# Kernel optimization log

Measured on AMD Instinct MI355X. Metric: run time of the kernel, lower is better.

The kernel has to match this reference:

```python
import jax, jax.numpy as jnp
import numpy as np

# Module constants (match init_kwargs)
M = 2049                      # NpointsMesh (odd)
TAU = 2.821e-5                # Gaussian spreading width ~ 12*(pi/M)^2
XLIMS = (0.0, 10.0)
L = abs(XLIMS[1] - XLIMS[0])
KGRID = jnp.asarray(np.linspace(-(M // 2), M // 2, M), dtype=jnp.float32)        # (M,)
XGRID = jnp.asarray(2.0 * np.pi * np.linspace(XLIMS[0], XLIMS[1], M + 1)[:-1] / L,
                    dtype=jnp.float32)                                           # (M,)
FOUR_PI = 4.0 * np.pi


def setup_inputs() -> dict:
    key = jax.random.key(0)
    kx, = jax.random.split(key, 1)
    x = jax.random.uniform(kx, (16, 1024), dtype=jnp.float32) * 10.0  # points in [xLims[0], xLims[1])
    ones = jnp.ones((1,), dtype=jnp.float32)  # tf.initializers.ones for all 4 weights
    return {"x": x, "shift0": ones, "amp0": ones, "shift1": ones, "amp1": ones}


def reference(x, shift0, amp0, shift1, amp1):
    # Gaussian spreading: (B, N, M)
    diff = x[..., None] * (2.0 * np.pi / L) - XGRID
    g = jnp.exp(-jnp.square(diff) / (4.0 * TAU))
    # Sum over points -> gridded density (B, M), then FFT + shift
    gsum = jnp.sum(g, axis=1).astype(jnp.complex64)
    fft_g = jnp.fft.fftshift(jnp.fft.fft(gsum, axis=-1), axes=-1) * (L / (2.0 * np.pi))
    # Deconvolution of the Gaussian kernel (real-valued)
    deconv = jnp.sqrt(np.pi / TAU) * jnp.exp(jnp.square(KGRID) * TAU)  # (M,)
    rfft = fft_g * deconv  # (B, M) complex
    # Fourier multipliers (real; imag parts are structurally zero in the original)
    m1 = -amp0 * FOUR_PI / (jnp.square(KGRID) + jnp.square(5.0 * shift0))            # (M,)
    m2 = amp1 * FOUR_PI * jnp.square(1.0 / (jnp.square(KGRID) + jnp.square(5.0 * shift1)))  # (M,)
    mult = jnp.stack([m1, m2], axis=0)  # (2, M)
    mult_fft = mult[None, :, :].astype(jnp.complex64) * rfft[:, None, :]  # (B, 2, M)
    mult_deconv = mult_fft * deconv  # second deconv application, as in the original
    # Inverse FFT back to the mesh, keep real part: (B, 2, M)
    irfft = jnp.real(jnp.fft.ifft(jnp.fft.ifftshift(mult_deconv, axes=-1), axis=-1))
    # Inverse interpolation back to the points: (B, N, 2, M) -> (B, N, 2)
    local = irfft[:, None, :, :] * g[:, :, None, :]
    fmm = jnp.sum(local, axis=-1) / M
    return fmm
```

## Files before the change

kernel.cpp:

```cpp
#include <hip/hip_runtime.h>
#include <math.h>

#define M_   2049
#define B_   16
#define N_   1024
#define TAU_ 2.821e-5
#define PI_  3.14159265358979323846
#define TWO_PI_ 6.283185307179586476925286766559

#define CV_SPLIT 16
#define MPAD     2052

#define GS_CH    8
#define HT_BLKS  33
#define FMM_QB   4

#define SW(i) ((i) + ((i) >> 2))

__global__ __launch_bounds__(256)
void spread_h3(const float* __restrict__ x,
               const float* __restrict__ s0, const float* __restrict__ a0,
               const float* __restrict__ s1, const float* __restrict__ a1,
               double* __restrict__ gsum_part, double* __restrict__ hhalf) {
    __shared__ double smem[4609];
    const int bx  = blockIdx.x;
    const int tid = threadIdx.x;

    if (bx < GS_CH * B_) {
        const int b  = bx >> 3;
        const int ch = bx & (GS_CH - 1);
        for (int i = tid; i < M_; i += 256) smem[i] = 0.0;
        __syncthreads();
        const int pl  = tid >> 1;
        const int sub = tid & 1;
        const double du      = TWO_PI_ / (double)M_;
        const double inv4tau = 1.0 / (4.0 * TAU_);
        const double xv = (double)x[(b << 10) + (ch << 7) + pl];
        const double u  = xv * (TWO_PI_ / 10.0);
        const int mc = (int)(xv * ((double)M_ / 10.0) + 0.5);
        const int start = mc - 33 + sub * 34;
        for (int i = 0; i < 34; ++i) {
            int m = start + i;
            if (m >= 0 && m < M_) {
                double d = u - du * (double)m;
                double t = d * d * inv4tau;
                if (t < 88.0) atomicAdd(&smem[m], (double)__expf(-(float)t));
            }
        }
        __syncthreads();
        double* gp = gsum_part + ((size_t)ch * B_ + b) * M_;
        for (int i = tid; i < M_; i += 256) gp[i] = smem[i];
    } else {
        const int dtile = bx - GS_CH * B_;
        double* costab = smem;
        double* cf0    = smem + 2049;
        double* cf1    = smem + 3073;
        double* red    = smem + 4097;
        const double ang0 = TWO_PI_ / (double)M_;
        for (int i = tid; i <= 1024; i += 256) {
            double v = cos(ang0 * (double)i);
            costab[i] = v;
            if (i > 0) costab[M_ - i] = v;
        }
        const double sA = 5.0 * (double)s0[0], sB = 5.0 * (double)s1[0];
        const double amp0 = (double)a0[0],     amp1 = (double)a1[0];
        for (int jj = tid; jj < 1024; jj += 256) {
            double j  = (double)(jj + 1);
            double k2 = j * j;
            double dec2 = (PI_ / TAU_) * exp(2.0 * TAU_ * k2);
            double base = 2.0 * (10.0 / TWO_PI_) * dec2 / (double)M_;
            cf0[jj] = base * (-amp0 * 4.0 * PI_ / (k2 + sA * sA));
            double den = k2 + sB * sB;
            cf1[jj] = base * (amp1 * 4.0 * PI_ / (den * den));
        }
        __syncthreads();
        const int dl = tid & 31;
        const int jq = tid >> 5;
        const int d  = (dtile << 5) + dl;
        double acc0 = 0.0, acc1 = 0.0;
        if (d <= 1024) {
            const int jlo = (jq << 7) + 1;
            int r = (int)(((long long)jlo * (long long)d) % M_);
            #pragma unroll 4
            for (int jj = 0; jj < 128; ++jj) {
                double cv_ = costab[r];
                acc0 += cf0[(jq << 7) + jj] * cv_;
                acc1 += cf1[(jq << 7) + jj] * cv_;
                r += d; if (r >= M_) r -= M_;
            }
        }
        red[tid]       = acc0;
        red[256 + tid] = acc1;
        __syncthreads();
        if (tid < 32) {
            const int dd = (dtile << 5) + tid;
            if (dd <= 1024) {
                const double w0base = (10.0 / TWO_PI_) * (PI_ / TAU_) / (double)M_;
                double h0 = w0base * (-amp0 * 4.0 * PI_ / (sA * sA));
                double h1 = w0base * (amp1 * 4.0 * PI_ / ((sB * sB) * (sB * sB)));
                #pragma unroll
                for (int q = 0; q < 8; ++q) {
                    h0 += red[(q << 5) + tid];
                    h1 += red[256 + (q << 5) + tid];
                }
                hhalf[dd]        = h0;
                hhalf[1025 + dd] = h1;
            }
        }
    }
}

__global__ void conv_kernel(const double* __restrict__ gsum_part,
                            const double* __restrict__ hhalf,
                            double* __restrict__ part) {
    __shared__ double w0s[1456];
    __shared__ double w1s[1456];
    __shared__ double red[512];
    __shared__ double gls[132];
    const int mt = blockIdx.x;
    const int s  = blockIdx.y;
    const int b  = blockIdx.z;
    const int m0  = mt * 1024;
    const int p0  = (s * M_) / CV_SPLIT;
    const int p1  = ((s + 1) * M_) / CV_SPLIT;
    const int len = p1 - p0;
    const int wcount = 1024 + len;
    int base = m0 - (p0 + len - 1);
    while (base < 0) base += M_;
    for (int i = threadIdx.x; i < wcount; i += 256) {
        int idx = base + i;
        while (idx >= M_) idx -= M_;
        int dd = (idx > 1024) ? (M_ - idx) : idx;
        w0s[SW(i)] = hhalf[dd];
        w1s[SW(i)] = hhalf[1025 + dd];
    }
    for (int i = threadIdx.x; i < len; i += 256) {
        double acc = 0.0;
        #pragma unroll
        for (int ch = 0; ch < GS_CH; ++ch)
            acc += gsum_part[((size_t)ch * B_ + b) * M_ + p0 + i];
        gls[i] = acc;
    }
    __syncthreads();

    const int q = 4 * threadIdx.x + len - 1;
    double A0 = w0s[SW(q)], A1 = w0s[SW(q+1)], A2 = w0s[SW(q+2)], A3 = w0s[SW(q+3)];
    double C0 = w1s[SW(q)], C1 = w1s[SW(q+1)], C2 = w1s[SW(q+2)], C3 = w1s[SW(q+3)];
    double a00=0.0,a01=0.0,a02=0.0,a03=0.0, a10=0.0,a11=0.0,a12=0.0,a13=0.0;
    int j = q, tt = 0;
    for (; tt + 4 <= len; tt += 4) {
        double g;
        g = gls[tt];
        a00 += g*A0; a01 += g*A1; a02 += g*A2; a03 += g*A3;
        a10 += g*C0; a11 += g*C1; a12 += g*C2; a13 += g*C3;
        A3 = w0s[SW(j-1)]; C3 = w1s[SW(j-1)];
        g = gls[tt+1];
        a00 += g*A3; a01 += g*A0; a02 += g*A1; a03 += g*A2;
        a10 += g*C3; a11 += g*C0; a12 += g*C1; a13 += g*C2;
        A2 = w0s[SW(j-2)]; C2 = w1s[SW(j-2)];
        g = gls[tt+2];
        a00 += g*A2; a01 += g*A3; a02 += g*A0; a03 += g*A1;
        a10 += g*C2; a11 += g*C3; a12 += g*C0; a13 += g*C1;
        A1 = w0s[SW(j-3)]; C1 = w1s[SW(j-3)];
        g = gls[tt+3];
        a00 += g*A1; a01 += g*A2; a02 += g*A3; a03 += g*A0;
        a10 += g*C1; a11 += g*C2; a12 += g*C3; a13 += g*C0;
        A0 = w0s[SW(j-4)]; C0 = w1s[SW(j-4)];
        j -= 4;
    }
    for (; tt < len; ++tt) {
        double g = gls[tt];
        a00 += g*A0; a01 += g*A1; a02 += g*A2; a03 += g*A3;
        a10 += g*C0; a11 += g*C1; a12 += g*C2; a13 += g*C3;
    }
    {
        double* pv = part + (((size_t)s * B_ + b) * 2) * MPAD + m0 + 4 * threadIdx.x;
        pv[0]        = a00; pv[1]        = a01; pv[2]        = a02; pv[3]        = a03;
        pv[MPAD + 0] = a10; pv[MPAD + 1] = a11; pv[MPAD + 2] = a12; pv[MPAD + 3] = a13;
    }
    if (mt == 1) {
        double t0 = 0.0, t1 = 0.0;
        if (threadIdx.x < len) {
            double g = gls[threadIdx.x];
            int qq = 1023 + len - threadIdx.x;
            t0 = g * w0s[SW(qq)];
            t1 = g * w1s[SW(qq)];
        }
        red[threadIdx.x]       = t0;
        red[256 + threadIdx.x] = t1;
        __syncthreads();
        for (int off = 128; off > 0; off >>= 1) {
            if (threadIdx.x < off) {
                red[threadIdx.x]       += red[threadIdx.x + off];
                red[256 + threadIdx.x] += red[256 + threadIdx.x + off];
            }
            __syncthreads();
        }
        if (threadIdx.x == 0) {
            double* pv = part + (((size_t)s * B_ + b) * 2) * MPAD;
            pv[2048]        = red[0];
            pv[MPAD + 2048] = red[256];
        }
    }
}

__global__ __launch_bounds__(256)
void reduce_fmm(const float* __restrict__ x, const double* __restrict__ part,
                float* __restrict__ out) {
    __shared__ double convs[2 * M_];
    const int b   = blockIdx.x >> 2;
    const int qb  = blockIdx.x & (FMM_QB - 1);
    const int tid = threadIdx.x;
    const size_t sstride = (size_t)B_ * 2 * MPAD;
    for (int ch = 0; ch < 2; ++ch) {
        const size_t off0 = ((size_t)b * 2 + ch) * MPAD;
        for (int m = tid; m < M_; m += 256) {
            double acc = 0.0;
            #pragma unroll
            for (int k = 0; k < CV_SPLIT; ++k)
                acc += part[(size_t)k * sstride + off0 + m];
            convs[ch * M_ + m] = acc;
        }
    }
    __syncthreads();
    const double du      = TWO_PI_ / (double)M_;
    const double inv4tau = 1.0 / (4.0 * TAU_);
    const int p  = (b << 10) + (qb << 8) + tid;
    const double xv = (double)x[p];
    const double u  = xv * (TWO_PI_ / 10.0);
    int mc = (int)(xv * ((double)M_ / 10.0) + 0.5);
    int lo = mc - 34; if (lo < 0) lo = 0;
    int hi = mc + 34; if (hi > M_ - 1) hi = M_ - 1;
    double av0 = 0.0, av1 = 0.0;
    for (int m = lo; m <= hi; ++m) {
        double d = u - du * (double)m;
        double g = (double)__expf(-(float)(d * d * inv4tau));
        av0 += g * convs[m];
        av1 += g * convs[M_ + m];
    }
    out[p * 2 + 0] = (float)(av0 / (double)M_);
    out[p * 2 + 1] = (float)(av1 / (double)M_);
}

extern "C" void kernel_launch(void* const* d_in, const int* in_sizes, int n_in,
                              void* d_out, int out_size, void* d_ws, size_t ws_size,
                              hipStream_t stream) {
    (void)in_sizes; (void)n_in; (void)out_size; (void)ws_size;
    const float* x  = (const float*)d_in[0];
    const float* s0 = (const float*)d_in[1];
    const float* a0 = (const float*)d_in[2];
    const float* s1 = (const float*)d_in[3];
    const float* a1 = (const float*)d_in[4];
    float* out = (float*)d_out;

    double* gsum_part = (double*)d_ws;
    double* hhalf     = gsum_part + GS_CH * B_ * M_;
    double* part      = hhalf + 2 * 1025;

    hipLaunchKernelGGL(spread_h3, dim3(GS_CH * B_ + HT_BLKS), dim3(256), 0, stream,
                       x, s0, a0, s1, a1, gsum_part, hhalf);
    hipLaunchKernelGGL(conv_kernel, dim3(2, CV_SPLIT, B_), dim3(256), 0, stream,
                       gsum_part, hhalf, part);
    hipLaunchKernelGGL(reduce_fmm, dim3(B_ * FMM_QB), dim3(256), 0, stream,
                       x, part, out);
}
```

Measured before the change: 97.79 us.

## Split reduce and gather kernels, widen parallelism, build cosine table by angle addition

```diff
diff --git a/kernel.cpp b/kernel.cpp
--- a/kernel.cpp
+++ b/kernel.cpp
@@ -12,17 +12,17 @@
 #define MPAD     2052
 
 #define GS_CH    8
-#define HT_BLKS  33
-#define FMM_QB   4
+#define HT_BLKS  65
+#define FMM_LPP  16
 
 #define SW(i) ((i) + ((i) >> 2))
 
 __global__ __launch_bounds__(256)
-void spread_h3(const float* __restrict__ x,
+void spread_h4(const float* __restrict__ x,
                const float* __restrict__ s0, const float* __restrict__ a0,
                const float* __restrict__ s1, const float* __restrict__ a1,
                double* __restrict__ gsum_part, double* __restrict__ hhalf) {
-    __shared__ double smem[4609];
+    __shared__ double smem[4803];
     const int bx  = blockIdx.x;
     const int tid = threadIdx.x;
 
@@ -56,11 +56,19 @@
         double* cf0    = smem + 2049;
         double* cf1    = smem + 3073;
         double* red    = smem + 4097;
-        const double ang0 = TWO_PI_ / (double)M_;
-        for (int i = tid; i <= 1024; i += 256) {
-            double v = cos(ang0 * (double)i);
-            costab[i] = v;
-            if (i > 0) costab[M_ - i] = v;
+        double* cc     = smem + 4609;
+        double* cs     = smem + 4642;
+        double* fc     = smem + 4675;
+        double* fs     = smem + 4739;
+        const double th = TWO_PI_ / (double)M_;
+        if (tid < 33) {
+            double a = th * 64.0 * (double)tid;
+            cc[tid] = cos(a);
+            cs[tid] = sin(a);
+        } else if (tid >= 64 && tid < 128) {
+            double a = th * (double)(tid - 64);
+            fc[tid - 64] = cos(a);
+            fs[tid - 64] = sin(a);
         }
         const double sA = 5.0 * (double)s0[0], sB = 5.0 * (double)s1[0];
         const double amp0 = (double)a0[0],     amp1 = (double)a1[0];
@@ -74,34 +82,39 @@
             cf1[jj] = base * (amp1 * 4.0 * PI_ / (den * den));
         }
         __syncthreads();
-        const int dl = tid & 31;
-        const int jq = tid >> 5;
-        const int d  = (dtile << 5) + dl;
+        for (int i = tid; i < M_; i += 256) {
+            int q = i >> 6, r = i & 63;
+            costab[i] = cc[q] * fc[r] - cs[q] * fs[r];
+        }
+        __syncthreads();
+        const int dl = tid & 15;
+        const int jq = tid >> 4;
+        const int d  = (dtile << 4) + dl;
         double acc0 = 0.0, acc1 = 0.0;
         if (d <= 1024) {
-            const int jlo = (jq << 7) + 1;
+            const int jlo = (jq << 6) + 1;
             int r = (int)(((long long)jlo * (long long)d) % M_);
             #pragma unroll 4
-            for (int jj = 0; jj < 128; ++jj) {
+            for (int jj = 0; jj < 64; ++jj) {
                 double cv_ = costab[r];
-                acc0 += cf0[(jq << 7) + jj] * cv_;
-                acc1 += cf1[(jq << 7) + jj] * cv_;
+                acc0 += cf0[(jq << 6) + jj] * cv_;
+                acc1 += cf1[(jq << 6) + jj] * cv_;
                 r += d; if (r >= M_) r -= M_;
             }
         }
         red[tid]       = acc0;
         red[256 + tid] = acc1;
         __syncthreads();
-        if (tid < 32) {
-            const int dd = (dtile << 5) + tid;
+        if (tid < 16) {
+            const int dd = (dtile << 4) + tid;
             if (dd <= 1024) {
                 const double w0base = (10.0 / TWO_PI_) * (PI_ / TAU_) / (double)M_;
                 double h0 = w0base * (-amp0 * 4.0 * PI_ / (sA * sA));
                 double h1 = w0base * (amp1 * 4.0 * PI_ / ((sB * sB) * (sB * sB)));
                 #pragma unroll
-                for (int q = 0; q < 8; ++q) {
-                    h0 += red[(q << 5) + tid];
-                    h1 += red[256 + (q << 5) + tid];
+                for (int q = 0; q < 16; ++q) {
+                    h0 += red[(q << 4) + tid];
+                    h1 += red[256 + (q << 4) + tid];
                 }
                 hhalf[dd]        = h0;
                 hhalf[1025 + dd] = h1;
@@ -204,42 +217,52 @@
     }
 }
 
-__global__ __launch_bounds__(256)
-void reduce_fmm(const float* __restrict__ x, const double* __restrict__ part,
-                float* __restrict__ out) {
-    __shared__ double convs[2 * M_];
-    const int b   = blockIdx.x >> 2;
-    const int qb  = blockIdx.x & (FMM_QB - 1);
-    const int tid = threadIdx.x;
+__global__ void reduce_kernel(const double* __restrict__ part, double* __restrict__ conv) {
+    const int idx = blockIdx.x * 256 + threadIdx.x;
+    if (idx >= B_ * 2 * M_) return;
+    const int b  = idx / (2 * M_);
+    const int rm = idx - b * 2 * M_;
+    const int c  = rm / M_;
+    const int m  = rm - c * M_;
+    const size_t off = ((size_t)b * 2 + c) * MPAD + m;
     const size_t sstride = (size_t)B_ * 2 * MPAD;
-    for (int ch = 0; ch < 2; ++ch) {
-        const size_t off0 = ((size_t)b * 2 + ch) * MPAD;
-        for (int m = tid; m < M_; m += 256) {
-            double acc = 0.0;
-            #pragma unroll
-            for (int k = 0; k < CV_SPLIT; ++k)
-                acc += part[(size_t)k * sstride + off0 + m];
-            convs[ch * M_ + m] = acc;
-        }
-    }
-    __syncthreads();
+    double acc = 0.0;
+    #pragma unroll
+    for (int k = 0; k < CV_SPLIT; ++k)
+        acc += part[(size_t)k * sstride + off];
+    conv[idx] = acc;
+}
+
+__global__ void fmm_kernel(const float* __restrict__ x, const double* __restrict__ conv,
+                           float* __restrict__ out) {
+    const int gid = blockIdx.x * 256 + threadIdx.x;
+    const int pt  = gid / FMM_LPP;
+    const int sub = gid % FMM_LPP;
+    const int b   = pt >> 10;
     const double du      = TWO_PI_ / (double)M_;
     const double inv4tau = 1.0 / (4.0 * TAU_);
-    const int p  = (b << 10) + (qb << 8) + tid;
-    const double xv = (double)x[p];
+    const double xv = (double)x[pt];
     const double u  = xv * (TWO_PI_ / 10.0);
     int mc = (int)(xv * ((double)M_ / 10.0) + 0.5);
     int lo = mc - 34; if (lo < 0) lo = 0;
     int hi = mc + 34; if (hi > M_ - 1) hi = M_ - 1;
-    double av0 = 0.0, av1 = 0.0;
-    for (int m = lo; m <= hi; ++m) {
+    const double* c0 = conv + (size_t)(b * 2) * M_;
+    const double* c1 = c0 + M_;
+    double a0 = 0.0, a1 = 0.0;
+    for (int m = lo + sub; m <= hi; m += FMM_LPP) {
         double d = u - du * (double)m;
         double g = (double)__expf(-(float)(d * d * inv4tau));
-        av0 += g * convs[m];
-        av1 += g * convs[M_ + m];
-    }
-    out[p * 2 + 0] = (float)(av0 / (double)M_);
-    out[p * 2 + 1] = (float)(av1 / (double)M_);
+        a0 += g * c0[m];
+        a1 += g * c1[m];
+    }
+    a0 += __shfl_xor(a0, 1); a1 += __shfl_xor(a1, 1);
+    a0 += __shfl_xor(a0, 2); a1 += __shfl_xor(a1, 2);
+    a0 += __shfl_xor(a0, 4); a1 += __shfl_xor(a1, 4);
+    a0 += __shfl_xor(a0, 8); a1 += __shfl_xor(a1, 8);
+    if (sub == 0) {
+        out[pt * 2 + 0] = (float)(a0 / (double)M_);
+        out[pt * 2 + 1] = (float)(a1 / (double)M_);
+    }
 }
 
 extern "C" void kernel_launch(void* const* d_in, const int* in_sizes, int n_in,
@@ -255,12 +278,15 @@
 
     double* gsum_part = (double*)d_ws;
     double* hhalf     = gsum_part + GS_CH * B_ * M_;
-    double* part      = hhalf + 2 * 1025;
-
-    hipLaunchKernelGGL(spread_h3, dim3(GS_CH * B_ + HT_BLKS), dim3(256), 0, stream,
+    double* conv      = hhalf + 2 * 1025;
+    double* part      = conv + B_ * 2 * M_;
+
+    hipLaunchKernelGGL(spread_h4, dim3(GS_CH * B_ + HT_BLKS), dim3(256), 0, stream,
                        x, s0, a0, s1, a1, gsum_part, hhalf);
     hipLaunchKernelGGL(conv_kernel, dim3(2, CV_SPLIT, B_), dim3(256), 0, stream,
                        gsum_part, hhalf, part);
-    hipLaunchKernelGGL(reduce_fmm, dim3(B_ * FMM_QB), dim3(256), 0, stream,
-                       x, part, out);
-}
+    hipLaunchKernelGGL(reduce_kernel, dim3((B_ * 2 * M_ + 255) / 256), dim3(256), 0, stream,
+                       part, conv);
+    hipLaunchKernelGGL(fmm_kernel, dim3(B_ * N_ * FMM_LPP / 256), dim3(256), 0, stream,
+                       x, conv, out);
+}
```

Measured after the change: 89.40 us (median of 2 runs). -8.6%, faster.
